# Kernel optimization log

Measured on AMD Instinct MI355X. Metric: run time of the kernel, lower is better.

## Reference

```python
import jax, jax.numpy as jnp
import numpy as np

N_CUMULANTS = 3  # forward() calls compute_cumulants_fwd(values, 3)
P = 576
N_ROWS = 200000
PROJ_DIMS = 4


def setup_inputs() -> dict:
    key = jax.random.key(0)
    k1, k2, k3 = jax.random.split(key, 3)
    X = jax.random.normal(k1, (N_ROWS, P), dtype=jnp.float32)
    mu = jax.random.normal(k2, (P * N_CUMULANTS,), dtype=jnp.float32)
    W = jax.random.normal(k3, (P * N_CUMULANTS, PROJ_DIMS), dtype=jnp.float32)
    return {"X": X, "mu": mu, "W": W}


def _cumulants(X):
    # X: (N, P). Vectorized version of the per-column torch loop.
    # n_cumulants = 3: c0 = mean, c1 = mean(centered^1), c2 = mean(centered^2)
    m = jnp.mean(X, axis=0)                 # (P,)
    centered = X - m                        # (N, P)
    mom1 = jnp.mean(centered, axis=0)       # (P,) ~0 numerically, kept for faithfulness
    mom2 = jnp.mean(centered * centered, axis=0)  # (P,) variance
    # layout matches out[:, jbase:jbase+n_cumulants]: interleave per feature column
    c = jnp.stack([m, mom1, mom2], axis=1)  # (P, 3)
    return c.reshape(1, -1)                 # (1, P*3)


def reference(X, mu, W):
    cum = _cumulants(X.astype(jnp.float32))          # (1, P*3)
    projected = jnp.einsum('ij,jk->ik', cum - mu, W)  # (1, PROJ_DIMS)
    return projected
```

## Files before the change

kernel.cpp:

```cpp
#include <hip/hip_runtime.h>

#define N_ROWS 200000
#define P 576
#define P4 144
#define GRID1 1024


__global__ __launch_bounds__(576) void colsum_kernel(const float4* __restrict__ X4,
                                                     float* __restrict__ S1,
                                                     float* __restrict__ S2) {
    const int x = threadIdx.x;
    const int y = threadIdx.y;

    float4 s1 = make_float4(0.f, 0.f, 0.f, 0.f);
    float4 s2 = make_float4(0.f, 0.f, 0.f, 0.f);

    for (int r = blockIdx.x * 4 + y; r < N_ROWS; r += GRID1 * 4) {
        float4 v = X4[(size_t)r * P4 + x];
        s1.x += v.x;      s1.y += v.y;      s1.z += v.z;      s1.w += v.w;
        s2.x += v.x * v.x; s2.y += v.y * v.y; s2.z += v.z * v.z; s2.w += v.w * v.w;
    }

    __shared__ float4 sh1[4][P4];
    __shared__ float4 sh2[4][P4];
    sh1[y][x] = s1;
    sh2[y][x] = s2;
    __syncthreads();

    if (y == 0) {
        #pragma unroll
        for (int i = 1; i < 4; ++i) {
            float4 a = sh1[i][x], b = sh2[i][x];
            s1.x += a.x; s1.y += a.y; s1.z += a.z; s1.w += a.w;
            s2.x += b.x; s2.y += b.y; s2.z += b.z; s2.w += b.w;
        }
        atomicAdd(&S1[4 * x + 0], s1.x);
        atomicAdd(&S1[4 * x + 1], s1.y);
        atomicAdd(&S1[4 * x + 2], s1.z);
        atomicAdd(&S1[4 * x + 3], s1.w);
        atomicAdd(&S2[4 * x + 0], s2.x);
        atomicAdd(&S2[4 * x + 1], s2.y);
        atomicAdd(&S2[4 * x + 2], s2.z);
        atomicAdd(&S2[4 * x + 3], s2.w);
    }
}

__global__ __launch_bounds__(256) void project_kernel(const float* __restrict__ S1,
                                                      const float* __restrict__ S2,
                                                      const float* __restrict__ mu,
                                                      const float* __restrict__ W,
                                                      float* __restrict__ out) {
    const int tid = threadIdx.x;
    const float invN = 1.0f / (float)N_ROWS;
    float acc0 = 0.f, acc1 = 0.f, acc2 = 0.f, acc3 = 0.f;

    for (int p = tid; p < P; p += 256) {
        float m    = S1[p] * invN;
        float mom2 = S2[p] * invN - m * m;
        int j = 3 * p;
        float c0 = m    - mu[j];
        float c1 = 0.f  - mu[j + 1];
        float c2 = mom2 - mu[j + 2];
        const float* w0 = &W[(size_t)j * 4];
        acc0 += c0 * w0[0] + c1 * w0[4] + c2 * w0[8];
        acc1 += c0 * w0[1] + c1 * w0[5] + c2 * w0[9];
        acc2 += c0 * w0[2] + c1 * w0[6] + c2 * w0[10];
        acc3 += c0 * w0[3] + c1 * w0[7] + c2 * w0[11];
    }

    #pragma unroll
    for (int off = 32; off > 0; off >>= 1) {
        acc0 += __shfl_down(acc0, off);
        acc1 += __shfl_down(acc1, off);
        acc2 += __shfl_down(acc2, off);
        acc3 += __shfl_down(acc3, off);
    }

    __shared__ float sacc[4][4];
    const int wave = tid >> 6;
    const int lane = tid & 63;
    if (lane == 0) {
        sacc[wave][0] = acc0;
        sacc[wave][1] = acc1;
        sacc[wave][2] = acc2;
        sacc[wave][3] = acc3;
    }
    __syncthreads();
    if (tid < 4) {
        float r = sacc[0][tid] + sacc[1][tid] + sacc[2][tid] + sacc[3][tid];
        out[tid] = r;
    }
}

extern "C" void kernel_launch(void* const* d_in, const int* in_sizes, int n_in,
                              void* d_out, int out_size, void* d_ws, size_t ws_size,
                              hipStream_t stream) {
    const float* X  = (const float*)d_in[0];
    const float* mu = (const float*)d_in[1];
    const float* W  = (const float*)d_in[2];
    float* out = (float*)d_out;

    float* S1 = (float*)d_ws;
    float* S2 = S1 + P;

    hipMemsetAsync(d_ws, 0, 2 * P * sizeof(float), stream);

    dim3 block(P4, 4);
    colsum_kernel<<<GRID1, block, 0, stream>>>((const float4*)X, S1, S2);
    project_kernel<<<1, 256, 0, stream>>>(S1, S2, mu, W, out);
}
```

Baseline: 649.9 us.

## Fuse projection into column-sum kernel via last-block ticket and unroll row loop

Merges the separate projection kernel into the column-sum kernel. The last block to finish, found through an atomic ticket counter, computes the cumulants and the 4-wide projection, which removes one kernel launch. The row loop now handles two rows per iteration into independent accumulators to get more loads in flight, and the grid shrinks from 1024 to 768 blocks. The cost is extra fences and syncthreads in every block, plus a serialized tail in the final block.

```diff
diff --git a/kernel.cpp b/kernel.cpp
--- a/kernel.cpp
+++ b/kernel.cpp
@@ -3,70 +3,99 @@
 #define N_ROWS 200000
 #define P 576
 #define P4 144
-#define GRID1 1024
+#define GRID1 768
+#define STRIPE (GRID1 * 8)
 
 
-__global__ __launch_bounds__(576) void colsum_kernel(const float4* __restrict__ X4,
-                                                     float* __restrict__ S1,
-                                                     float* __restrict__ S2) {
+__global__ __launch_bounds__(576) void colsum_project_kernel(
+    const float4* __restrict__ X4,
+    const float*  __restrict__ mu,
+    const float*  __restrict__ W,
+    float*        __restrict__ S1,
+    float*        __restrict__ S2,
+    unsigned int* __restrict__ ticket,
+    float*        __restrict__ out)
+{
     const int x = threadIdx.x;
     const int y = threadIdx.y;
 
-    float4 s1 = make_float4(0.f, 0.f, 0.f, 0.f);
-    float4 s2 = make_float4(0.f, 0.f, 0.f, 0.f);
+    float4 s1a = make_float4(0.f, 0.f, 0.f, 0.f);
+    float4 s2a = make_float4(0.f, 0.f, 0.f, 0.f);
+    float4 s1b = make_float4(0.f, 0.f, 0.f, 0.f);
+    float4 s2b = make_float4(0.f, 0.f, 0.f, 0.f);
 
-    for (int r = blockIdx.x * 4 + y; r < N_ROWS; r += GRID1 * 4) {
+    for (int r = blockIdx.x * 8 + y; r < N_ROWS; r += STRIPE) {
         float4 v = X4[(size_t)r * P4 + x];
-        s1.x += v.x;      s1.y += v.y;      s1.z += v.z;      s1.w += v.w;
-        s2.x += v.x * v.x; s2.y += v.y * v.y; s2.z += v.z * v.z; s2.w += v.w * v.w;
+        s1a.x += v.x;  s1a.y += v.y;  s1a.z += v.z;  s1a.w += v.w;
+        s2a.x = fmaf(v.x, v.x, s2a.x);
+        s2a.y = fmaf(v.y, v.y, s2a.y);
+        s2a.z = fmaf(v.z, v.z, s2a.z);
+        s2a.w = fmaf(v.w, v.w, s2a.w);
+
+        const int r2 = r + 4;
+        if (r2 < N_ROWS) {
+            float4 w = X4[(size_t)r2 * P4 + x];
+            s1b.x += w.x;  s1b.y += w.y;  s1b.z += w.z;  s1b.w += w.w;
+            s2b.x = fmaf(w.x, w.x, s2b.x);
+            s2b.y = fmaf(w.y, w.y, s2b.y);
+            s2b.z = fmaf(w.z, w.z, s2b.z);
+            s2b.w = fmaf(w.w, w.w, s2b.w);
+        }
     }
+
+    s1a.x += s1b.x; s1a.y += s1b.y; s1a.z += s1b.z; s1a.w += s1b.w;
+    s2a.x += s2b.x; s2a.y += s2b.y; s2a.z += s2b.z; s2a.w += s2b.w;
 
     __shared__ float4 sh1[4][P4];
     __shared__ float4 sh2[4][P4];
-    sh1[y][x] = s1;
-    sh2[y][x] = s2;
+    sh1[y][x] = s1a;
+    sh2[y][x] = s2a;
     __syncthreads();
 
     if (y == 0) {
         #pragma unroll
         for (int i = 1; i < 4; ++i) {
             float4 a = sh1[i][x], b = sh2[i][x];
-            s1.x += a.x; s1.y += a.y; s1.z += a.z; s1.w += a.w;
-            s2.x += b.x; s2.y += b.y; s2.z += b.z; s2.w += b.w;
+            s1a.x += a.x; s1a.y += a.y; s1a.z += a.z; s1a.w += a.w;
+            s2a.x += b.x; s2a.y += b.y; s2a.z += b.z; s2a.w += b.w;
         }
-        atomicAdd(&S1[4 * x + 0], s1.x);
-        atomicAdd(&S1[4 * x + 1], s1.y);
-        atomicAdd(&S1[4 * x + 2], s1.z);
-        atomicAdd(&S1[4 * x + 3], s1.w);
-        atomicAdd(&S2[4 * x + 0], s2.x);
-        atomicAdd(&S2[4 * x + 1], s2.y);
-        atomicAdd(&S2[4 * x + 2], s2.z);
-        atomicAdd(&S2[4 * x + 3], s2.w);
+        atomicAdd(&S1[4 * x + 0], s1a.x);
+        atomicAdd(&S1[4 * x + 1], s1a.y);
+        atomicAdd(&S1[4 * x + 2], s1a.z);
+        atomicAdd(&S1[4 * x + 3], s1a.w);
+        atomicAdd(&S2[4 * x + 0], s2a.x);
+        atomicAdd(&S2[4 * x + 1], s2a.y);
+        atomicAdd(&S2[4 * x + 2], s2a.z);
+        atomicAdd(&S2[4 * x + 3], s2a.w);
     }
-}
 
-__global__ __launch_bounds__(256) void project_kernel(const float* __restrict__ S1,
-                                                      const float* __restrict__ S2,
-                                                      const float* __restrict__ mu,
-                                                      const float* __restrict__ W,
-                                                      float* __restrict__ out) {
-    const int tid = threadIdx.x;
+    __shared__ int isLast;
+    __syncthreads();
+    const int tid = y * P4 + x;
+    if (tid == 0) {
+        __threadfence();
+        unsigned int t = atomicAdd(ticket, 1u);
+        isLast = (t == GRID1 - 1);
+    }
+    __syncthreads();
+    if (!isLast) return;
+    __threadfence();
+
     const float invN = 1.0f / (float)N_ROWS;
-    float acc0 = 0.f, acc1 = 0.f, acc2 = 0.f, acc3 = 0.f;
+    float s1v = __hip_atomic_load(&S1[tid], __ATOMIC_RELAXED, __HIP_MEMORY_SCOPE_AGENT);
+    float s2v = __hip_atomic_load(&S2[tid], __ATOMIC_RELAXED, __HIP_MEMORY_SCOPE_AGENT);
+    float m    = s1v * invN;
+    float mom2 = s2v * invN - m * m;
 
-    for (int p = tid; p < P; p += 256) {
-        float m    = S1[p] * invN;
-        float mom2 = S2[p] * invN - m * m;
-        int j = 3 * p;
-        float c0 = m    - mu[j];
-        float c1 = 0.f  - mu[j + 1];
-        float c2 = mom2 - mu[j + 2];
-        const float* w0 = &W[(size_t)j * 4];
-        acc0 += c0 * w0[0] + c1 * w0[4] + c2 * w0[8];
-        acc1 += c0 * w0[1] + c1 * w0[5] + c2 * w0[9];
-        acc2 += c0 * w0[2] + c1 * w0[6] + c2 * w0[10];
-        acc3 += c0 * w0[3] + c1 * w0[7] + c2 * w0[11];
-    }
+    const int j = 3 * tid;
+    float c0 = m    - mu[j];
+    float c1 = 0.f  - mu[j + 1];
+    float c2 = mom2 - mu[j + 2];
+    const float* w0 = &W[(size_t)j * 4];
+    float acc0 = c0 * w0[0] + c1 * w0[4] + c2 * w0[8];
+    float acc1 = c0 * w0[1] + c1 * w0[5] + c2 * w0[9];
+    float acc2 = c0 * w0[2] + c1 * w0[6] + c2 * w0[10];
+    float acc3 = c0 * w0[3] + c1 * w0[7] + c2 * w0[11];
 
     #pragma unroll
     for (int off = 32; off > 0; off >>= 1) {
@@ -76,7 +105,7 @@
         acc3 += __shfl_down(acc3, off);
     }
 
-    __shared__ float sacc[4][4];
+    __shared__ float sacc[9][4];
     const int wave = tid >> 6;
     const int lane = tid & 63;
     if (lane == 0) {
@@ -87,7 +116,9 @@
     }
     __syncthreads();
     if (tid < 4) {
-        float r = sacc[0][tid] + sacc[1][tid] + sacc[2][tid] + sacc[3][tid];
+        float r = 0.f;
+        #pragma unroll
+        for (int i = 0; i < 9; ++i) r += sacc[i][tid];
         out[tid] = r;
     }
 }
@@ -102,10 +133,11 @@
 
     float* S1 = (float*)d_ws;
     float* S2 = S1 + P;
+    unsigned int* ticket = (unsigned int*)(S2 + P);
 
-    hipMemsetAsync(d_ws, 0, 2 * P * sizeof(float), stream);
+    hipMemsetAsync(d_ws, 0, 2 * P * sizeof(float) + sizeof(unsigned int), stream);
 
     dim3 block(P4, 4);
-    colsum_kernel<<<GRID1, block, 0, stream>>>((const float4*)X, S1, S2);
-    project_kernel<<<1, 256, 0, stream>>>(S1, S2, mu, W, out);
+    colsum_project_kernel<<<GRID1, block, 0, stream>>>((const float4*)X, mu, W,
+                                                       S1, S2, ticket, out);
 }
```

New measurement: 643.1 us. About the same (-1.0%).
